# Optimization experiments

Hardware: AMD Instinct MI355X
Metric: run time of the kernel (lower is better)

Reference implementation:

```python
import jax, jax.numpy as jnp
import numpy as np

MAX_SOURCE_LEN = 2048
HIDDEN = 1024
HEADS = 16
NUM_BUCKETS = 32
MAX_DISTANCE = 128
LN_EPS = 1e-5


def relative_position_bucket(relative_position, num_buckets=NUM_BUCKETS, max_distance=MAX_DISTANCE):
    # Bidirectional T5-style bucketing.
    n = -relative_position
    half = num_buckets // 2
    ret = (n < 0).astype(jnp.int32) * half
    n = jnp.abs(n)
    max_exact = half // 2
    is_small = n < max_exact
    scale = (half - max_exact) / np.log(max_distance / max_exact)
    val_large = max_exact + (jnp.log(jnp.maximum(n, 1).astype(jnp.float32) / max_exact) * scale).astype(jnp.int32)
    val_large = jnp.minimum(val_large, half - 1)
    return ret + jnp.where(is_small, n.astype(jnp.int32), val_large)


def setup_inputs() -> dict:
    key = jax.random.key(0)
    ks = jax.random.split(key, 6)
    B, L = 4, 1024
    leaf_idx = jax.random.randint(ks[0], (B, L), 0, MAX_SOURCE_LEN)
    p_emb = jax.random.normal(ks[1], (MAX_SOURCE_LEN, HIDDEN), jnp.float32) * 0.02
    p_emb = p_emb.at[0].set(0.0)  # padding_idx=0
    r_emb = jax.random.normal(ks[2], (NUM_BUCKETS + 1, HEADS), jnp.float32) * 0.02
    r_emb = r_emb.at[NUM_BUCKETS].set(0.0)  # padding_idx=num_buckets
    Wq = jax.random.normal(ks[3], (HIDDEN, HIDDEN), jnp.float32) / np.sqrt(HIDDEN)
    Wk = jax.random.normal(ks[4], (HIDDEN, HIDDEN), jnp.float32) / np.sqrt(HIDDEN)
    return {
        "leaf_idx": leaf_idx,
        "p_emb": p_emb,
        "r_emb": r_emb,
        "ln_g": jnp.ones((HIDDEN,), jnp.float32),
        "ln_b": jnp.zeros((HIDDEN,), jnp.float32),
        "Wq": Wq,
        "bq": jnp.zeros((HIDDEN,), jnp.float32),
        "Wk": Wk,
        "bk": jnp.zeros((HIDDEN,), jnp.float32),
    }


def reference(leaf_idx, p_emb, r_emb, ln_g, ln_b, Wq, bq, Wk, bk):
    B, L = leaf_idx.shape
    H = r_emb.shape[1]
    d_k = p_emb.shape[1] // H

    # --- T5 relative-position bias ---
    # rel[b,i,j] = leaf[b,j] - leaf[b,i]  (matches unsqueeze(1) - unsqueeze(-1))
    rel = leaf_idx[:, None, :] - leaf_idx[:, :, None]
    bucket = relative_position_bucket(rel)
    valid = leaf_idx != 0
    pair = valid[:, None, :] & valid[:, :, None]
    bucket = jnp.where(pair, bucket, NUM_BUCKETS)
    t5_score = jnp.transpose(r_emb[bucket], (0, 3, 1, 2))  # [B,H,L,L]

    # --- untied position score ---
    x = p_emb[leaf_idx]  # [B,L,D]
    mu = jnp.mean(x, axis=-1, keepdims=True)
    var = jnp.mean(jnp.square(x - mu), axis=-1, keepdims=True)
    xn = (x - mu) * jax.lax.rsqrt(var + LN_EPS) * ln_g + ln_b

    q = (xn @ Wq.T + bq).reshape(B, L, H, d_k).transpose(0, 2, 1, 3) / np.sqrt(d_k)
    k = (xn @ Wk.T + bk).reshape(B, L, H, d_k).transpose(0, 2, 1, 3)
    untied = jnp.einsum("bhid,bhjd->bhij", q, k)

    return untied + t5_score  # leaf_PE_Type == 'Merge'
```

## Files before the change

kernel.cpp:

```cpp
#include <hip/hip_runtime.h>
#include <hip/hip_bf16.h>

typedef __attribute__((ext_vector_type(8))) short short8;
typedef __attribute__((ext_vector_type(4))) float f32x4;

#define L 1024
#define D 1024
#define NHEADS 16

static __device__ __forceinline__ unsigned short f2bf(float f) {
  union { float f; unsigned int u; } c; c.f = f;
  unsigned int u = c.u;
  u += 0x7fffu + ((u >> 16) & 1u);
  return (unsigned short)(u >> 16);
}

static __device__ __forceinline__ void gload_lds16(const void* gsrc, void* ldst) {
  __builtin_amdgcn_global_load_lds(
      (const __attribute__((address_space(1))) void*)gsrc,
      (__attribute__((address_space(3))) void*)ldst, 16, 0, 0);
}

__global__ __launch_bounds__(256) void prep_kernel(const int* __restrict__ leaf,
                                                   const float* __restrict__ p_emb,
                                                   const float* __restrict__ g,
                                                   const float* __restrict__ bcoef,
                                                   const float* __restrict__ Wq,
                                                   const float* __restrict__ Wk,
                                                   unsigned short* __restrict__ w,
                                                   unsigned short* __restrict__ xn,
                                                   unsigned char* __restrict__ bucket) {
  int bid = blockIdx.x;
  int t = threadIdx.x;
  if (bid < 2048) {
    int idx = bid * 256 + t;
    bool isq = (idx < 262144);
    const float* src = isq ? Wq : Wk;
    float sc = isq ? 0.125f : 1.0f;
    int rel = isq ? idx : idx - 262144;
    float4 v = ((const float4*)src)[rel];
    ushort4 o;
    o.x = f2bf(v.x * sc); o.y = f2bf(v.y * sc); o.z = f2bf(v.z * sc); o.w = f2bf(v.w * sc);
    ((ushort4*)w)[idx] = o;
  } else if (bid < 6144) {
    int row = bid - 2048;
    int lane = t & 63, wv = t >> 6;
    int leafv = leaf[row];
    float4 xv = ((const float4*)(p_emb + (size_t)leafv * D))[t];
    float s  = xv.x + xv.y + xv.z + xv.w;
    float s2 = xv.x*xv.x + xv.y*xv.y + xv.z*xv.z + xv.w*xv.w;
    #pragma unroll
    for (int o = 1; o < 64; o <<= 1) {
      s  += __shfl_xor(s, o);
      s2 += __shfl_xor(s2, o);
    }
    __shared__ float red[8];
    if (lane == 0) { red[wv*2] = s; red[wv*2+1] = s2; }
    __syncthreads();
    float st  = red[0] + red[2] + red[4] + red[6];
    float s2t = red[1] + red[3] + red[5] + red[7];
    float mu = st * (1.0f/1024.0f);
    float var = s2t * (1.0f/1024.0f) - mu*mu;
    float rs = rsqrtf(var + 1e-5f);
    float4 gv = ((const float4*)g)[t];
    float4 bv = ((const float4*)bcoef)[t];
    ushort4 o;
    o.x = f2bf((xv.x - mu) * rs * gv.x + bv.x);
    o.y = f2bf((xv.y - mu) * rs * gv.y + bv.y);
    o.z = f2bf((xv.z - mu) * rs * gv.z + bv.z);
    o.w = f2bf((xv.w - mu) * rs * gv.w + bv.w);
    ((ushort4*)xn)[row * 256 + t] = o;
  } else {
    int idx = (bid - 6144) * 256 + t;
    int j = idx & 1023;
    int rest = idx >> 10;
    int i = rest & 1023;
    int b = rest >> 10;
    int li = leaf[b * L + i];
    int lj = leaf[b * L + j];
    int n = li - lj;
    int ret = 0;
    if (n < 0) { ret = 16; n = -n; }
    int val;
    if (n < 8) {
      val = n;
    } else {
      val = 8 + (int)(logf((float)n * 0.125f) * 2.8853900817779268f);
      if (val > 15) val = 15;
    }
    val += ret;
    if (li == 0 || lj == 0) val = 32;
    bucket[idx] = (unsigned char)val;
  }
}

__global__ __launch_bounds__(256) void qk_gemm_kernel(const unsigned short* __restrict__ xn,
                                                      const unsigned short* __restrict__ wqk,
                                                      const float* __restrict__ bq,
                                                      const float* __restrict__ bk,
                                                      unsigned short* __restrict__ qws,
                                                      unsigned short* __restrict__ kws) {
  __shared__ __align__(16) unsigned short As[2][128 * 32];
  __shared__ __align__(16) unsigned short Bs[2][64 * 32];
  int t = threadIdx.x;
  int lane = t & 63, w = t >> 6;
  int wr = w >> 1, wc = w & 1;
  int wg = blockIdx.x;
  int swz = (wg & 7) * 128 + (wg >> 3);
  int m0 = (swz >> 5) * 128;
  int n0 = (swz & 31) * 64;

  f32x4 acc[4][2] = {};

  auto stage = [&](int buf, int kt) {
    int k0 = kt * 32;
    #pragma unroll
    for (int r = 0; r < 2; ++r) {
      int c = t + r * 256;
      int row = c >> 2, kc = c & 3;
      gload_lds16(xn + (size_t)(m0 + row) * D + k0 + kc * 8, &As[buf][c * 8]);
    }
    {
      int row = t >> 2, kc = t & 3;
      gload_lds16(wqk + (size_t)(n0 + row) * D + k0 + kc * 8, &Bs[buf][t * 8]);
    }
  };

  stage(0, 0);
  __syncthreads();
  for (int kt = 0; kt < 32; ++kt) {
    int cur = kt & 1;
    if (kt < 31) stage(cur ^ 1, kt + 1);
    short8 a[4], b[2];
    #pragma unroll
    for (int f = 0; f < 4; ++f) {
      int arow = wr * 64 + f * 16 + (lane & 15);
      a[f] = *(const short8*)&As[cur][arow * 32 + (lane >> 4) * 8];
    }
    #pragma unroll
    for (int f = 0; f < 2; ++f) {
      int brow = wc * 32 + f * 16 + (lane & 15);
      b[f] = *(const short8*)&Bs[cur][brow * 32 + (lane >> 4) * 8];
    }
    #pragma unroll
    for (int i = 0; i < 4; ++i)
      #pragma unroll
      for (int j = 0; j < 2; ++j)
        acc[i][j] = __builtin_amdgcn_mfma_f32_16x16x32_bf16(b[j], a[i], acc[i][j], 0, 0, 0);
    __syncthreads();
  }

  bool isq = (n0 < 1024);
  const float* bias = isq ? bq : bk;
  float scale = isq ? 0.125f : 1.0f;
  unsigned short* outp = isq ? qws : kws;
  int nbase = n0 - (isq ? 0 : 1024);

  float4 bv[2];
  #pragma unroll
  for (int j = 0; j < 2; ++j) {
    bv[j] = *(const float4*)(bias + nbase + wc * 32 + j * 16 + (lane >> 4) * 4);
    bv[j].x *= scale; bv[j].y *= scale; bv[j].z *= scale; bv[j].w *= scale;
  }

  #pragma unroll
  for (int i = 0; i < 4; ++i) {
    int m = m0 + wr * 64 + i * 16 + (lane & 15);
    int bb = m >> 10, ii = m & 1023;
    #pragma unroll
    for (int j = 0; j < 2; ++j) {
      int n0c = nbase + wc * 32 + j * 16 + (lane >> 4) * 4;
      int h = n0c >> 6, k0 = n0c & 63;
      int bh = bb * NHEADS + h;
      unsigned p0 = (unsigned)f2bf(acc[i][j][0] + bv[j].x) | ((unsigned)f2bf(acc[i][j][1] + bv[j].y) << 16);
      unsigned p1 = (unsigned)f2bf(acc[i][j][2] + bv[j].z) | ((unsigned)f2bf(acc[i][j][3] + bv[j].w) << 16);
      size_t off = (size_t)bh * 65536 + (size_t)(ii >> 4) * 1024
                 + (size_t)(k0 >> 3) * 128 + (ii & 15) * 8 + (k0 & 7);
      uint2 pv; pv.x = p0; pv.y = p1;
      *(uint2*)(outp + off) = pv;
    }
  }
}

__global__ __launch_bounds__(256) void untied_kernel(const unsigned short* __restrict__ qws,
                                                     const unsigned short* __restrict__ kws,
                                                     const unsigned char* __restrict__ bucket,
                                                     const float* __restrict__ r_emb,
                                                     float* __restrict__ out) {
  __shared__ float rt[33 * 17];
  __shared__ __align__(16) unsigned char bt[128 * 128];
  int t = threadIdx.x;
  for (int idx = t; idx < 528; idx += 256)
    rt[(idx >> 4) * 17 + (idx & 15)] = r_emb[idx];

  int bid = blockIdx.x;
  int lg = (bid & 7) * 512 + (bid >> 3);
  int h  = lg & 15;
  int jt = (lg >> 4) & 7;
  int it = (lg >> 7) & 7;
  int b  = lg >> 10;
  int lane = t & 63, w = t >> 6;
  int wr = w >> 1, wc = w & 1;
  int i0 = it * 128, j0 = jt * 128;
  int bh = b * NHEADS + h;

  const unsigned char* bsrc = bucket + (size_t)b * L * L + (size_t)i0 * L + j0;
  {
    #pragma unroll
    for (int iter = 0; iter < 4; ++iter) {
      int lofs = iter * 4096 + w * 1024 + lane * 16;
      int row = lofs >> 7;
      int cb = (lofs >> 4) & 7;
      gload_lds16(bsrc + (size_t)row * L + (size_t)((cb ^ (row & 7)) << 4), &bt[lofs]);
    }
  }

  const unsigned short* qb = qws + (size_t)bh * 65536;
  const unsigned short* kb = kws + (size_t)bh * 65536;

  short8 a[4][2], bf[4][2];
  #pragma unroll
  for (int f = 0; f < 4; ++f) {
    #pragma unroll
    for (int ks = 0; ks < 2; ++ks) {
      a[f][ks]  = *(const short8*)(qb + (size_t)(i0 / 16 + wr * 4 + f) * 1024 + ks * 512 + lane * 8);
      bf[f][ks] = *(const short8*)(kb + (size_t)(j0 / 16 + wc * 4 + f) * 1024 + ks * 512 + lane * 8);
    }
  }

  __syncthreads();

  f32x4 acc[4][4] = {};
  #pragma unroll
  for (int ks = 0; ks < 2; ++ks)
    #pragma unroll
    for (int i = 0; i < 4; ++i)
      #pragma unroll
      for (int j = 0; j < 4; ++j)
        acc[i][j] = __builtin_amdgcn_mfma_f32_16x16x32_bf16(bf[j][ks], a[i][ks], acc[i][j], 0, 0, 0);

  unsigned bw[4][4];
  #pragma unroll
  for (int i = 0; i < 4; ++i) {
    int il = wr * 64 + i * 16 + (lane & 15);
    #pragma unroll
    for (int j = 0; j < 4; ++j) {
      int jl = wc * 64 + j * 16 + (lane >> 4) * 4;
      int jd = jl >> 2;
      int addr = il * 128 + (((jd >> 2) ^ (il & 7)) << 4) + ((jd & 3) << 2);
      bw[i][j] = *(const unsigned*)&bt[addr];
    }
  }

  float* ob = out + (size_t)bh * L * L;
  const float* rth = rt + h;
  #pragma unroll
  for (int i = 0; i < 4; ++i) {
    int il = wr * 64 + i * 16 + (lane & 15);
    #pragma unroll
    for (int j = 0; j < 4; ++j) {
      int jl = wc * 64 + j * 16 + (lane >> 4) * 4;
      unsigned w32 = bw[i][j];
      float4 o;
      o.x = acc[i][j][0] + rth[(w32 & 255u) * 17];
      o.y = acc[i][j][1] + rth[((w32 >> 8) & 255u) * 17];
      o.z = acc[i][j][2] + rth[((w32 >> 16) & 255u) * 17];
      o.w = acc[i][j][3] + rth[(w32 >> 24) * 17];
      *(float4*)(ob + (size_t)(i0 + il) * L + (j0 + jl)) = o;
    }
  }
}

extern "C" void kernel_launch(void* const* d_in, const int* in_sizes, int n_in,
                              void* d_out, int out_size, void* d_ws, size_t ws_size,
                              hipStream_t stream) {
  const int*   leaf  = (const int*)d_in[0];
  const float* p_emb = (const float*)d_in[1];
  const float* r_emb = (const float*)d_in[2];
  const float* ln_g  = (const float*)d_in[3];
  const float* ln_b  = (const float*)d_in[4];
  const float* Wq    = (const float*)d_in[5];
  const float* bq    = (const float*)d_in[6];
  const float* Wk    = (const float*)d_in[7];
  const float* bk    = (const float*)d_in[8];
  float* out = (float*)d_out;

  char* ws = (char*)d_ws;
  unsigned short* xn   = (unsigned short*)(ws);
  unsigned short* wqk  = (unsigned short*)(ws + (8u  << 20));
  unsigned short* qws  = (unsigned short*)(ws + (12u << 20));
  unsigned short* kws  = (unsigned short*)(ws + (20u << 20));
  unsigned char*  bckt = (unsigned char*)(ws + (28u << 20));

  prep_kernel<<<22528, 256, 0, stream>>>(leaf, p_emb, ln_g, ln_b, Wq, Wk, wqk, xn, bckt);
  qk_gemm_kernel<<<1024, 256, 0, stream>>>(xn, wqk, bq, bk, qws, kws);
  untied_kernel<<<4096, 256, 0, stream>>>(qws, kws, bckt, r_emb, out);
}
```

Measured before the change: 105.8 us.

## Enlarge QK GEMM tile to 128x128x64 with XOR-swizzled LDS and nontemporal output stores

The Q/K projection GEMM moves from 128x64 tiles with K-step 32 to 128x128 tiles with K-step 64, halving the grid to 512 blocks. LDS rows are XOR-swizzled to avoid bank conflicts on the wider rows. Each wave now holds 4x4 accumulators, which raises arithmetic intensity per load at the cost of more registers and LDS and fewer blocks. The untied kernel's final fp32 output writes become nontemporal stores so the large output does not pollute the cache.

New measurement: 128.7 us. 21.7% more time.

```diff
diff --git a/kernel.cpp b/kernel.cpp
--- a/kernel.cpp
+++ b/kernel.cpp
@@ -100,53 +100,58 @@
                                                       const float* __restrict__ bk,
                                                       unsigned short* __restrict__ qws,
                                                       unsigned short* __restrict__ kws) {
-  __shared__ __align__(16) unsigned short As[2][128 * 32];
-  __shared__ __align__(16) unsigned short Bs[2][64 * 32];
+  __shared__ __align__(16) unsigned short As[2][128 * 64];
+  __shared__ __align__(16) unsigned short Bs[2][128 * 64];
   int t = threadIdx.x;
   int lane = t & 63, w = t >> 6;
   int wr = w >> 1, wc = w & 1;
   int wg = blockIdx.x;
-  int swz = (wg & 7) * 128 + (wg >> 3);
-  int m0 = (swz >> 5) * 128;
-  int n0 = (swz & 31) * 64;
-
-  f32x4 acc[4][2] = {};
+  int swz = (wg & 7) * 64 + (wg >> 3);
+  int m0 = (swz >> 4) * 128;
+  int n0 = (swz & 15) * 128;
+
+  f32x4 acc[4][4] = {};
 
   auto stage = [&](int buf, int kt) {
-    int k0 = kt * 32;
-    #pragma unroll
-    for (int r = 0; r < 2; ++r) {
-      int c = t + r * 256;
-      int row = c >> 2, kc = c & 3;
-      gload_lds16(xn + (size_t)(m0 + row) * D + k0 + kc * 8, &As[buf][c * 8]);
-    }
-    {
-      int row = t >> 2, kc = t & 3;
-      gload_lds16(wqk + (size_t)(n0 + row) * D + k0 + kc * 8, &Bs[buf][t * 8]);
+    int k0 = kt * 64;
+    #pragma unroll
+    for (int r = 0; r < 4; ++r) {
+      int lofs = r * 4096 + t * 16;
+      int row = lofs >> 7;
+      int c = (lofs >> 4) & 7;
+      int cs = c ^ (row & 7);
+      gload_lds16(xn + (size_t)(m0 + row) * D + k0 + cs * 8,
+                  (char*)As[buf] + lofs);
+      gload_lds16(wqk + (size_t)(n0 + row) * D + k0 + cs * 8,
+                  (char*)Bs[buf] + lofs);
     }
   };
 
   stage(0, 0);
   __syncthreads();
-  for (int kt = 0; kt < 32; ++kt) {
+  for (int kt = 0; kt < 16; ++kt) {
     int cur = kt & 1;
-    if (kt < 31) stage(cur ^ 1, kt + 1);
-    short8 a[4], b[2];
+    if (kt < 15) stage(cur ^ 1, kt + 1);
+    short8 a[4][2], b[4][2];
     #pragma unroll
     for (int f = 0; f < 4; ++f) {
       int arow = wr * 64 + f * 16 + (lane & 15);
-      a[f] = *(const short8*)&As[cur][arow * 32 + (lane >> 4) * 8];
-    }
-    #pragma unroll
-    for (int f = 0; f < 2; ++f) {
-      int brow = wc * 32 + f * 16 + (lane & 15);
-      b[f] = *(const short8*)&Bs[cur][brow * 32 + (lane >> 4) * 8];
-    }
-    #pragma unroll
-    for (int i = 0; i < 4; ++i)
+      int brow = wc * 64 + f * 16 + (lane & 15);
       #pragma unroll
-      for (int j = 0; j < 2; ++j)
-        acc[i][j] = __builtin_amdgcn_mfma_f32_16x16x32_bf16(b[j], a[i], acc[i][j], 0, 0, 0);
+      for (int ks = 0; ks < 2; ++ks) {
+        int ca = (ks * 4 + (lane >> 4)) ^ (arow & 7);
+        int cb = (ks * 4 + (lane >> 4)) ^ (brow & 7);
+        a[f][ks] = *(const short8*)&As[cur][arow * 64 + ca * 8];
+        b[f][ks] = *(const short8*)&Bs[cur][brow * 64 + cb * 8];
+      }
+    }
+    #pragma unroll
+    for (int ks = 0; ks < 2; ++ks)
+      #pragma unroll
+      for (int i = 0; i < 4; ++i)
+        #pragma unroll
+        for (int j = 0; j < 4; ++j)
+          acc[i][j] = __builtin_amdgcn_mfma_f32_16x16x32_bf16(b[j][ks], a[i][ks], acc[i][j], 0, 0, 0);
     __syncthreads();
   }
 
@@ -156,10 +161,10 @@
   unsigned short* outp = isq ? qws : kws;
   int nbase = n0 - (isq ? 0 : 1024);
 
-  float4 bv[2];
-  #pragma unroll
-  for (int j = 0; j < 2; ++j) {
-    bv[j] = *(const float4*)(bias + nbase + wc * 32 + j * 16 + (lane >> 4) * 4);
+  float4 bv[4];
+  #pragma unroll
+  for (int j = 0; j < 4; ++j) {
+    bv[j] = *(const float4*)(bias + nbase + wc * 64 + j * 16 + (lane >> 4) * 4);
     bv[j].x *= scale; bv[j].y *= scale; bv[j].z *= scale; bv[j].w *= scale;
   }
 
@@ -168,8 +173,8 @@
     int m = m0 + wr * 64 + i * 16 + (lane & 15);
     int bb = m >> 10, ii = m & 1023;
     #pragma unroll
-    for (int j = 0; j < 2; ++j) {
-      int n0c = nbase + wc * 32 + j * 16 + (lane >> 4) * 4;
+    for (int j = 0; j < 4; ++j) {
+      int n0c = nbase + wc * 64 + j * 16 + (lane >> 4) * 4;
       int h = n0c >> 6, k0 = n0c & 63;
       int bh = bb * NHEADS + h;
       unsigned p0 = (unsigned)f2bf(acc[i][j][0] + bv[j].x) | ((unsigned)f2bf(acc[i][j][1] + bv[j].y) << 16);
@@ -261,12 +266,12 @@
     for (int j = 0; j < 4; ++j) {
       int jl = wc * 64 + j * 16 + (lane >> 4) * 4;
       unsigned w32 = bw[i][j];
-      float4 o;
-      o.x = acc[i][j][0] + rth[(w32 & 255u) * 17];
-      o.y = acc[i][j][1] + rth[((w32 >> 8) & 255u) * 17];
-      o.z = acc[i][j][2] + rth[((w32 >> 16) & 255u) * 17];
-      o.w = acc[i][j][3] + rth[(w32 >> 24) * 17];
-      *(float4*)(ob + (size_t)(i0 + il) * L + (j0 + jl)) = o;
+      f32x4 o = acc[i][j];
+      o[0] += rth[(w32 & 255u) * 17];
+      o[1] += rth[((w32 >> 8) & 255u) * 17];
+      o[2] += rth[((w32 >> 16) & 255u) * 17];
+      o[3] += rth[(w32 >> 24) * 17];
+      __builtin_nontemporal_store(o, (f32x4*)(ob + (size_t)(i0 + il) * L + (j0 + jl)));
     }
   }
 }
@@ -293,6 +298,6 @@
   unsigned char*  bckt = (unsigned char*)(ws + (28u << 20));
 
   prep_kernel<<<22528, 256, 0, stream>>>(leaf, p_emb, ln_g, ln_b, Wq, Wk, wqk, xn, bckt);
-  qk_gemm_kernel<<<1024, 256, 0, stream>>>(xn, wqk, bq, bk, qws, kws);
+  qk_gemm_kernel<<<512, 256, 0, stream>>>(xn, wqk, bq, bk, qws, kws);
   untied_kernel<<<4096, 256, 0, stream>>>(qws, kws, bckt, r_emb, out);
 }
```

## Compute T5 buckets inline in untied kernel instead of materializing bucket tensor

Applied to the files above, without the earlier changes.

Drops the bucket-precompute phase of the prep kernel, which wrote a 4M-byte bucket array, and the untied kernel's async load of that array into LDS. Each untied block now loads its 128 row and 128 column leaf indices into LDS and computes the bucket per element, including a logf, in the epilogue. This removes a global write and read pass plus many prep blocks, in exchange for recomputing buckets for all 16 heads (16x redundant ALU work with transcendentals).

Result: slower. 113.2 us (+7.0%).

```diff
diff --git a/kernel.cpp b/kernel.cpp
--- a/kernel.cpp
+++ b/kernel.cpp
@@ -19,6 +19,22 @@
   __builtin_amdgcn_global_load_lds(
       (const __attribute__((address_space(1))) void*)gsrc,
       (__attribute__((address_space(3))) void*)ldst, 16, 0, 0);
+}
+
+static __device__ __forceinline__ int t5_bucket(int li, int lj) {
+  int n = li - lj;
+  int ret = 0;
+  if (n < 0) { ret = 16; n = -n; }
+  int val;
+  if (n < 8) {
+    val = n;
+  } else {
+    val = 8 + (int)(logf((float)n * 0.125f) * 2.8853900817779268f);
+    if (val > 15) val = 15;
+  }
+  val += ret;
+  if (li == 0 || lj == 0) val = 32;
+  return val;
 }
 
 __global__ __launch_bounds__(256) void prep_kernel(const int* __restrict__ leaf,
@@ -28,8 +44,7 @@
                                                    const float* __restrict__ Wq,
                                                    const float* __restrict__ Wk,
                                                    unsigned short* __restrict__ w,
-                                                   unsigned short* __restrict__ xn,
-                                                   unsigned char* __restrict__ bucket) {
+                                                   unsigned short* __restrict__ xn) {
   int bid = blockIdx.x;
   int t = threadIdx.x;
   if (bid < 2048) {
@@ -42,7 +57,7 @@
     ushort4 o;
     o.x = f2bf(v.x * sc); o.y = f2bf(v.y * sc); o.z = f2bf(v.z * sc); o.w = f2bf(v.w * sc);
     ((ushort4*)w)[idx] = o;
-  } else if (bid < 6144) {
+  } else {
     int row = bid - 2048;
     int lane = t & 63, wv = t >> 6;
     int leafv = leaf[row];
@@ -70,27 +85,6 @@
     o.z = f2bf((xv.z - mu) * rs * gv.z + bv.z);
     o.w = f2bf((xv.w - mu) * rs * gv.w + bv.w);
     ((ushort4*)xn)[row * 256 + t] = o;
-  } else {
-    int idx = (bid - 6144) * 256 + t;
-    int j = idx & 1023;
-    int rest = idx >> 10;
-    int i = rest & 1023;
-    int b = rest >> 10;
-    int li = leaf[b * L + i];
-    int lj = leaf[b * L + j];
-    int n = li - lj;
-    int ret = 0;
-    if (n < 0) { ret = 16; n = -n; }
-    int val;
-    if (n < 8) {
-      val = n;
-    } else {
-      val = 8 + (int)(logf((float)n * 0.125f) * 2.8853900817779268f);
-      if (val > 15) val = 15;
-    }
-    val += ret;
-    if (li == 0 || lj == 0) val = 32;
-    bucket[idx] = (unsigned char)val;
   }
 }
 
@@ -184,11 +178,12 @@
 
 __global__ __launch_bounds__(256) void untied_kernel(const unsigned short* __restrict__ qws,
                                                      const unsigned short* __restrict__ kws,
-                                                     const unsigned char* __restrict__ bucket,
+                                                     const int* __restrict__ leaf,
                                                      const float* __restrict__ r_emb,
                                                      float* __restrict__ out) {
   __shared__ float rt[33 * 17];
-  __shared__ __align__(16) unsigned char bt[128 * 128];
+  __shared__ __align__(16) int lI[128];
+  __shared__ __align__(16) int lJ[128];
   int t = threadIdx.x;
   for (int idx = t; idx < 528; idx += 256)
     rt[(idx >> 4) * 17 + (idx & 15)] = r_emb[idx];
@@ -204,16 +199,8 @@
   int i0 = it * 128, j0 = jt * 128;
   int bh = b * NHEADS + h;
 
-  const unsigned char* bsrc = bucket + (size_t)b * L * L + (size_t)i0 * L + j0;
-  {
-    #pragma unroll
-    for (int iter = 0; iter < 4; ++iter) {
-      int lofs = iter * 4096 + w * 1024 + lane * 16;
-      int row = lofs >> 7;
-      int cb = (lofs >> 4) & 7;
-      gload_lds16(bsrc + (size_t)row * L + (size_t)((cb ^ (row & 7)) << 4), &bt[lofs]);
-    }
-  }
+  if (t < 128) lI[t] = leaf[b * L + i0 + t];
+  else         lJ[t - 128] = leaf[b * L + j0 + (t - 128)];
 
   const unsigned short* qb = qws + (size_t)bh * 65536;
   const unsigned short* kb = kws + (size_t)bh * 65536;
@@ -239,34 +226,22 @@
       for (int j = 0; j < 4; ++j)
         acc[i][j] = __builtin_amdgcn_mfma_f32_16x16x32_bf16(bf[j][ks], a[i][ks], acc[i][j], 0, 0, 0);
 
-  unsigned bw[4][4];
+  float* ob = out + (size_t)bh * L * L;
+  const float* rth = rt + h;
   #pragma unroll
   for (int i = 0; i < 4; ++i) {
     int il = wr * 64 + i * 16 + (lane & 15);
+    int li = lI[il];
     #pragma unroll
     for (int j = 0; j < 4; ++j) {
       int jl = wc * 64 + j * 16 + (lane >> 4) * 4;
-      int jd = jl >> 2;
-      int addr = il * 128 + (((jd >> 2) ^ (il & 7)) << 4) + ((jd & 3) << 2);
-      bw[i][j] = *(const unsigned*)&bt[addr];
-    }
-  }
-
-  float* ob = out + (size_t)bh * L * L;
-  const float* rth = rt + h;
-  #pragma unroll
-  for (int i = 0; i < 4; ++i) {
-    int il = wr * 64 + i * 16 + (lane & 15);
-    #pragma unroll
-    for (int j = 0; j < 4; ++j) {
-      int jl = wc * 64 + j * 16 + (lane >> 4) * 4;
-      unsigned w32 = bw[i][j];
-      float4 o;
-      o.x = acc[i][j][0] + rth[(w32 & 255u) * 17];
-      o.y = acc[i][j][1] + rth[((w32 >> 8) & 255u) * 17];
-      o.z = acc[i][j][2] + rth[((w32 >> 16) & 255u) * 17];
-      o.w = acc[i][j][3] + rth[(w32 >> 24) * 17];
-      *(float4*)(ob + (size_t)(i0 + il) * L + (j0 + jl)) = o;
+      int4 ljv = *(const int4*)&lJ[jl];
+      f32x4 o = acc[i][j];
+      o[0] += rth[t5_bucket(li, ljv.x) * 17];
+      o[1] += rth[t5_bucket(li, ljv.y) * 17];
+      o[2] += rth[t5_bucket(li, ljv.z) * 17];
+      o[3] += rth[t5_bucket(li, ljv.w) * 17];
+      *(f32x4*)(ob + (size_t)(i0 + il) * L + (j0 + jl)) = o;
     }
   }
 }
@@ -290,9 +265,8 @@
   unsigned short* wqk  = (unsigned short*)(ws + (8u  << 20));
   unsigned short* qws  = (unsigned short*)(ws + (12u << 20));
   unsigned short* kws  = (unsigned short*)(ws + (20u << 20));
-  unsigned char*  bckt = (unsigned char*)(ws + (28u << 20));
-
-  prep_kernel<<<22528, 256, 0, stream>>>(leaf, p_emb, ln_g, ln_b, Wq, Wk, wqk, xn, bckt);
+
+  prep_kernel<<<6144, 256, 0, stream>>>(leaf, p_emb, ln_g, ln_b, Wq, Wk, wqk, xn);
   qk_gemm_kernel<<<1024, 256, 0, stream>>>(xn, wqk, bq, bk, qws, kws);
-  untied_kernel<<<4096, 256, 0, stream>>>(qws, kws, bckt, r_emb, out);
-}
+  untied_kernel<<<4096, 256, 0, stream>>>(qws, kws, leaf, r_emb, out);
+}
```
